# Performance work log

Hardware: AMD Instinct MI355X
Metric: run time of the kernel (lower is better)

Reference implementation:

```python
import jax, jax.numpy as jnp
import numpy as np

NUM_HEADS = 16
NUM_BUCKETS = 32
MAX_DISTANCE = 128


def _relative_position_bucket(relative_position, num_buckets=NUM_BUCKETS, max_distance=MAX_DISTANCE):
    # bidirectional=True (encoder self-attention)
    nb = num_buckets // 2  # 16
    buckets = (relative_position > 0).astype(jnp.int32) * nb
    rp = jnp.abs(relative_position)
    max_exact = nb // 2  # 8
    is_small = rp < max_exact
    # log-spaced bins for large distances; clamp arg of log to >=1 to avoid log(0)
    rp_f = jnp.maximum(rp, 1).astype(jnp.float32)
    large = max_exact + (
        jnp.log(rp_f / max_exact) / np.log(max_distance / max_exact) * (nb - max_exact)
    ).astype(jnp.int32)
    large = jnp.minimum(large, nb - 1)
    return buckets + jnp.where(is_small, rp, large)


def setup_inputs() -> dict:
    key = jax.random.key(0)
    ks = jax.random.split(key, 6)
    B, L, D = 2, 2048, 1024
    scale = 0.02  # keep activations in a sane range
    return {
        "hidden_states": jax.random.normal(ks[0], (B, L, D), dtype=jnp.float32),
        "Wq": jax.random.normal(ks[1], (D, D), dtype=jnp.float32) * scale,
        "Wk": jax.random.normal(ks[2], (D, D), dtype=jnp.float32) * scale,
        "Wv": jax.random.normal(ks[3], (D, D), dtype=jnp.float32) * scale,
        "Wo": jax.random.normal(ks[4], (D, D), dtype=jnp.float32) * scale,
        "bias_table": jax.random.normal(ks[5], (NUM_BUCKETS, NUM_HEADS), dtype=jnp.float32),
    }


def reference(hidden_states, Wq, Wk, Wv, Wo, bias_table):
    B, L, D = hidden_states.shape
    H = NUM_HEADS
    hd = D // H

    # projections (nn.Linear: y = x @ W.T), split heads -> [B, H, L, hd]
    def proj(x, W):
        return (x @ W.T).reshape(B, L, H, hd).transpose(0, 2, 1, 3)

    q = proj(hidden_states, Wq)
    k = proj(hidden_states, Wk)
    v = proj(hidden_states, Wv)

    # T5 relative position bias: [1, H, L, L]
    ctx = jnp.arange(L)[:, None]
    mem = jnp.arange(L)[None, :]
    buckets = _relative_position_bucket(mem - ctx)  # [L, L]
    position_bias = bias_table[buckets].transpose(2, 0, 1)[None]  # [1, H, L, L]

    # NOTE: T5-style attention has NO 1/sqrt(hd) scaling
    scores = jnp.einsum("bhqd,bhkd->bhqk", q, k) + position_bias
    attn = jax.nn.softmax(scores.astype(jnp.float32), axis=-1).astype(scores.dtype)
    out = jnp.einsum("bhqk,bhkd->bhqd", attn, v)
    out = out.transpose(0, 2, 1, 3).reshape(B, L, D)
    out = out @ Wo.T
    return out, position_bias
```

## Files before the change

kernel.cpp:

```cpp
#include <hip/hip_runtime.h>
#include <cstdint>
#include <cmath>

typedef unsigned short ushort_t;
typedef __bf16 bf16x8 __attribute__((ext_vector_type(8)));
typedef float f32x4 __attribute__((ext_vector_type(4)));
typedef ushort_t us4 __attribute__((ext_vector_type(4)));
typedef ushort_t us8 __attribute__((ext_vector_type(8)));

#define MFMA16(a, b, c) __builtin_amdgcn_mfma_f32_16x16x32_bf16(a, b, c, 0, 0, 0)
#define LOG2E 1.4426950408889634f

__device__ __forceinline__ ushort_t f2bf(float f) {
    union { __bf16 h; ushort_t u; } cv;
    cv.h = (__bf16)f;
    return cv.u;
}

__device__ __forceinline__ void glds16(const ushort_t* g, ushort_t* s) {
    __builtin_amdgcn_global_load_lds(
        (const __attribute__((address_space(1))) void*)(g),
        (__attribute__((address_space(3))) void*)(s), 16, 0, 0);
}

__global__ void cast_all_k(const float* __restrict__ x, const float* __restrict__ wq,
                           const float* __restrict__ wk, const float* __restrict__ wv,
                           const float* __restrict__ wo, ushort_t* __restrict__ xb,
                           ushort_t* __restrict__ wb, unsigned char* __restrict__ lut) {
    int id = blockIdx.x, t = threadIdx.x;
    if (id == 8192) {
        for (int idx = t; idx < 4095; idx += 256) {
            int rel = idx - 2047;
            int bb = (rel > 0) ? 16 : 0;
            int rp = (rel < 0) ? -rel : rel;
            int add;
            if (rp < 8) {
                add = rp;
            } else {
                float lg = (float)::log((double)rp * 0.125);
                double tt = ((double)lg) / 2.772588722239781 * 8.0;
                int large = 8 + (int)tt;
                add = (large < 15) ? large : 15;
            }
            lut[idx] = (unsigned char)(bb + add);
        }
        return;
    }
    const float* src;
    ushort_t* dst;
    int idx;
    float scale = 1.0f;
    if (id < 4096) {
        src = x; dst = xb; idx = id * 256 + t;
    } else {
        int r = (id - 4096) >> 10;
        idx = ((id - 4096) & 1023) * 256 + t;
        src = (r == 0) ? wq : (r == 1) ? wk : (r == 2) ? wv : wo;
        dst = wb + (size_t)r * 1048576;
        if (r == 0) scale = LOG2E;
    }
    float4 v = ((const float4*)src)[idx];
    us4 o;
    o.x = f2bf(v.x * scale); o.y = f2bf(v.y * scale);
    o.z = f2bf(v.z * scale); o.w = f2bf(v.w * scale);
    ((us4*)dst)[idx] = o;
}

template <int MODE>
__global__ __launch_bounds__(256) void gemm_bt_k(const ushort_t* __restrict__ A,
                                                 const ushort_t* __restrict__ B0,
                                                 void* __restrict__ C0,
                                                 int M, int N, int K, long sB, long sC) {
    __shared__ ushort_t As[128 * 64];
    __shared__ ushort_t Bs[128 * 64];
    const int tid = threadIdx.x;
    const int l = tid & 63, w = tid >> 6;
    const int quad = l >> 4, lc = l & 15;
    const int wm = w >> 1, wn = w & 1;
    const int m0 = blockIdx.y * 128, n0 = blockIdx.x * 128;
    const ushort_t* B = B0 + (long)blockIdx.z * sB;

    f32x4 acc[4][4] = {};
    const int rA = l >> 3;
    const int cA = ((l & 7) ^ rA) * 8;

    for (int k0 = 0; k0 < K; k0 += 64) {
#pragma unroll
        for (int t = 0; t < 4; ++t) {
            int row = w * 32 + t * 8;
            glds16(A + (size_t)(m0 + row + rA) * K + k0 + cA, &As[row * 64]);
            glds16(B + (size_t)(n0 + row + rA) * K + k0 + cA, &Bs[row * 64]);
        }
        __syncthreads();
#pragma unroll
        for (int ko = 0; ko < 2; ++ko) {
            const int ch = (((ko * 4 + quad) ^ (lc & 7))) * 8;
            bf16x8 af[4], bfr[4];
#pragma unroll
            for (int mt = 0; mt < 4; ++mt)
                af[mt] = *(const bf16x8*)&As[(wm * 64 + mt * 16 + lc) * 64 + ch];
#pragma unroll
            for (int nt = 0; nt < 4; ++nt)
                bfr[nt] = *(const bf16x8*)&Bs[(wn * 64 + nt * 16 + lc) * 64 + ch];
#pragma unroll
            for (int mt = 0; mt < 4; ++mt)
#pragma unroll
                for (int nt = 0; nt < 4; ++nt)
                    acc[mt][nt] = MFMA16(af[mt], bfr[nt], acc[mt][nt]);
        }
        __syncthreads();
    }
#pragma unroll
    for (int mt = 0; mt < 4; ++mt) {
#pragma unroll
        for (int nt = 0; nt < 4; ++nt) {
            int col = n0 + wn * 64 + nt * 16 + lc;
#pragma unroll
            for (int r = 0; r < 4; ++r) {
                int row = m0 + wm * 64 + mt * 16 + quad * 4 + r;
                if constexpr (MODE == 1) {
                    ((float*)C0)[(size_t)row * N + col] = acc[mt][nt][r];
                } else if constexpr (MODE == 0) {
                    (((ushort_t*)C0) + (long)blockIdx.z * sC)[(size_t)row * N + col] = f2bf(acc[mt][nt][r]);
                } else {
                    ((ushort_t*)C0)[(size_t)(col >> 11) * 2097152 + (size_t)row * 2048 + (col & 2047)] =
                        f2bf(acc[mt][nt][r]);
                }
            }
        }
    }
}

__global__ __launch_bounds__(256, 3) void attn_k(const ushort_t* __restrict__ Qg,
                                                 const ushort_t* __restrict__ Kg,
                                                 const ushort_t* __restrict__ VTg,
                                                 ushort_t* __restrict__ Ctx,
                                                 const unsigned char* __restrict__ lut,
                                                 const float* __restrict__ table,
                                                 float* __restrict__ bias_out) {
    __shared__ ushort_t Ks[128 * 64];
    __shared__ ushort_t VTs[64 * 128];
    __shared__ ushort_t QP[128 * 64];
    __shared__ float biasb[256];
    __shared__ float biasraw[256];

    const int tid = threadIdx.x, l = tid & 63, w = tid >> 6;
    const int quad = l >> 4, lc = l & 15;
    const int id = blockIdx.x;
    const int bh = id & 31, b = bh >> 4, h = bh & 15;
    const int q0 = (id >> 5) * 128;
    const size_t tokbase = (size_t)b * 2048;

    const int rK = l >> 3;
    const int cK = ((l & 7) ^ rK) * 8;
    const int rV = l >> 4;
    const int cVi = l & 15;

#pragma unroll
    for (int t = 0; t < 4; ++t) {
        int row0 = w * 32 + t * 8;
        glds16(Qg + (tokbase + q0 + row0 + rK) * 1024 + h * 64 + cK, &QP[row0 * 64]);
        glds16(Kg + (tokbase + row0 + rK) * 1024 + h * 64 + cK, &Ks[row0 * 64]);
    }
#pragma unroll
    for (int t = 0; t < 4; ++t) {
        int row0 = w * 16 + t * 4;
        int rsw = ((t & 1) * 4 + rV) & 7;
        int csw = (cVi & 8) | ((cVi & 7) ^ rsw);
        glds16(VTg + (size_t)(b * 1024 + h * 64 + row0 + rV) * 2048 + csw * 8, &VTs[row0 * 128]);
    }
    if (tid < 255) {
        float bvv = table[(int)lut[0 - q0 + tid + 1920] * 16 + h];
        biasraw[tid] = bvv;
        biasb[tid] = bvv * LOG2E;
    }
    __syncthreads();

    bf16x8 qf[2][2];
#pragma unroll
    for (int nt = 0; nt < 2; ++nt)
#pragma unroll
        for (int ko = 0; ko < 2; ++ko) {
            int row = w * 32 + nt * 16 + lc;
            int ch = ((ko * 4 + quad) ^ (lc & 7)) * 8;
            qf[nt][ko] = *(const bf16x8*)&QP[row * 64 + ch];
        }
    __syncthreads();

    float mstate[2] = {-1e30f, -1e30f};
    float lstate[2] = {0.f, 0.f};
    f32x4 acco[4][2] = {};
    ushort_t* Pw = &QP[w * 1280];
    const int cb0 = quad * 4 - (w * 32 + lc) + 127;
    const int cxor = lc & 3;

    const int bjf = (tid & 15) * 4 + b * 64;
    const int big = tid >> 4;

    for (int kt = 0; kt < 16; ++kt) {
        const int j0 = kt * 128;
        f32x4 accs[8][2] = {};
#pragma unroll
        for (int ko = 0; ko < 2; ++ko) {
            const int ch = ((ko * 4 + quad) ^ (lc & 7)) * 8;
#pragma unroll
            for (int mt = 0; mt < 8; ++mt) {
                bf16x8 kf = *(const bf16x8*)&Ks[(mt * 16 + lc) * 64 + ch];
                accs[mt][0] = MFMA16(kf, qf[0][ko], accs[mt][0]);
                accs[mt][1] = MFMA16(kf, qf[1][ko], accs[mt][1]);
            }
        }
        {
            float* outp = bias_out + ((size_t)h * 2048 + q0) * 2048 + j0;
#pragma unroll
            for (int rr = 0; rr < 8; ++rr) {
                int il = big + 16 * rr;
                int d0 = bjf - il + 127;
                f32x4 v;
                v[0] = biasraw[d0]; v[1] = biasraw[d0 + 1];
                v[2] = biasraw[d0 + 2]; v[3] = biasraw[d0 + 3];
                __builtin_nontemporal_store(v, (f32x4*)(outp + (size_t)il * 2048 + bjf));
            }
        }
        f32x4 bvp;
#pragma unroll
        for (int r = 0; r < 4; ++r) bvp[r] = biasb[cb0 - 16 + r];
#pragma unroll
        for (int mt = 0; mt < 8; ++mt) {
            f32x4 bvc;
#pragma unroll
            for (int r = 0; r < 4; ++r) bvc[r] = biasb[cb0 + mt * 16 + r];
            accs[mt][0] += bvc;
            accs[mt][1] += bvp;
            bvp = bvc;
        }
#pragma unroll
        for (int nt = 0; nt < 2; ++nt) {
            float mx = accs[0][nt][0];
#pragma unroll
            for (int mt = 0; mt < 8; ++mt)
#pragma unroll
                for (int r = 0; r < 4; ++r) mx = fmaxf(mx, accs[mt][nt][r]);
            mx = fmaxf(mx, __shfl_xor(mx, 16, 64));
            mx = fmaxf(mx, __shfl_xor(mx, 32, 64));
            float mo = mstate[nt], mn = fmaxf(mo, mx);
            float alpha = __builtin_amdgcn_exp2f(mo - mn);
            mstate[nt] = mn;
            float rs = 0.f;
#pragma unroll
            for (int mt = 0; mt < 8; ++mt)
#pragma unroll
                for (int r = 0; r < 4; ++r) {
                    float p = __builtin_amdgcn_exp2f(accs[mt][nt][r] - mn);
                    accs[mt][nt][r] = p;
                    rs += p;
                }
            rs += __shfl_xor(rs, 16, 64);
            rs += __shfl_xor(rs, 32, 64);
            lstate[nt] = lstate[nt] * alpha + rs;
#pragma unroll
            for (int dt = 0; dt < 4; ++dt) acco[dt][nt] *= alpha;
        }
#pragma unroll
        for (int kk = 0; kk < 4; ++kk) {
#pragma unroll
            for (int half = 0; half < 2; ++half) {
                int mt = kk * 2 + half;
                int c = half * 2 + (quad >> 1);
                int coff = ((c ^ cxor) * 8 + (quad & 1) * 4);
#pragma unroll
                for (int nt = 0; nt < 2; ++nt) {
                    us4 o;
#pragma unroll
                    for (int r = 0; r < 4; ++r) o[r] = f2bf(accs[mt][nt][r]);
                    *(us4*)&Pw[(nt * 16 + lc) * 40 + coff] = o;
                }
            }
            bf16x8 pf[2];
#pragma unroll
            for (int nt = 0; nt < 2; ++nt)
                pf[nt] = *(const bf16x8*)&Pw[(nt * 16 + lc) * 40 + (quad ^ cxor) * 8];
            bf16x8 vf[4];
#pragma unroll
            for (int dt = 0; dt < 4; ++dt) {
                int ch = kk * 4 + quad;
                int chs = ((ch & 8) | ((ch & 7) ^ (lc & 7))) * 8;
                vf[dt] = *(const bf16x8*)&VTs[(dt * 16 + lc) * 128 + chs];
            }
#pragma unroll
            for (int dt = 0; dt < 4; ++dt)
#pragma unroll
                for (int nt = 0; nt < 2; ++nt)
                    acco[dt][nt] = MFMA16(vf[dt], pf[nt], acco[dt][nt]);
        }
        __syncthreads();
        if (kt < 15) {
            const int jn = j0 + 128;
#pragma unroll
            for (int t = 0; t < 4; ++t) {
                int row0 = w * 32 + t * 8;
                glds16(Kg + (tokbase + jn + row0 + rK) * 1024 + h * 64 + cK, &Ks[row0 * 64]);
            }
#pragma unroll
            for (int t = 0; t < 4; ++t) {
                int row0 = w * 16 + t * 4;
                int rsw = ((t & 1) * 4 + rV) & 7;
                int csw = (cVi & 8) | ((cVi & 7) ^ rsw);
                glds16(VTg + (size_t)(b * 1024 + h * 64 + row0 + rV) * 2048 + jn + csw * 8,
                       &VTs[row0 * 128]);
            }
            if (tid < 255) {
                float bvv = table[(int)lut[jn - q0 + tid + 1920] * 16 + h];
                biasraw[tid] = bvv;
                biasb[tid] = bvv * LOG2E;
            }
            __syncthreads();
        }
    }
#pragma unroll
    for (int nt = 0; nt < 2; ++nt) {
        float inv = 1.0f / lstate[nt];
        size_t row = tokbase + q0 + w * 32 + nt * 16 + lc;
#pragma unroll
        for (int dt = 0; dt < 4; ++dt) {
            us4 o;
#pragma unroll
            for (int r = 0; r < 4; ++r) o[r] = f2bf(acco[dt][nt][r] * inv);
            *(us4*)&Ctx[row * 1024 + h * 64 + dt * 16 + quad * 4] = o;
        }
    }
}

extern "C" void kernel_launch(void* const* d_in, const int* in_sizes, int n_in,
                              void* d_out, int out_size, void* d_ws, size_t ws_size,
                              hipStream_t stream) {
    const float* hidden = (const float*)d_in[0];
    const float* Wq = (const float*)d_in[1];
    const float* Wk = (const float*)d_in[2];
    const float* Wv = (const float*)d_in[3];
    const float* Wo = (const float*)d_in[4];
    const float* table = (const float*)d_in[5];

    char* ws = (char*)d_ws;
    ushort_t* Xb  = (ushort_t*)(ws);
    ushort_t* Wb  = (ushort_t*)(ws + 8388608);
    ushort_t* Qg  = (ushort_t*)(ws + 16777216);
    ushort_t* Kgp = (ushort_t*)(ws + 25165824);
    ushort_t* VTg = (ushort_t*)(ws + 33554432);
    ushort_t* Ctx = (ushort_t*)(ws + 41943040);
    unsigned char* lutp = (unsigned char*)(ws + 50331648);

    float* out0 = (float*)d_out;
    float* out1 = out0 + 4194304;

    cast_all_k<<<8193, 256, 0, stream>>>(hidden, Wq, Wk, Wv, Wo, Xb, Wb, lutp);

    gemm_bt_k<0><<<dim3(8, 32, 2), 256, 0, stream>>>(Xb, Wb, (void*)Qg,
                                                     4096, 1024, 1024, 1048576, 4194304);
    gemm_bt_k<2><<<dim3(32, 8, 1), 256, 0, stream>>>(Wb + 2097152, Xb, (void*)VTg,
                                                     1024, 4096, 1024, 0, 0);
    attn_k<<<dim3(512), 256, 0, stream>>>(Qg, Kgp, VTg, Ctx, lutp, table, out1);
    gemm_bt_k<1><<<dim3(8, 32, 1), 256, 0, stream>>>(Ctx, Wb + 3145728, (void*)out0,
                                                     4096, 1024, 1024, 0, 0);
}
```

Baseline: 461.9 us.

## Double-buffer K tiles, load V fragments directly from global, single sync per tile

The attention kernel now double-buffers K tiles and the per-tile bias diagonal in shared memory, so loads for the next tile are issued before computing the current one. That replaces the two barriers per iteration with one. V^T fragments are read straight from global memory into registers at the start of each tile instead of being staged through LDS. The LOG2E scaling is folded into fmaf. Occupancy hint drops from 3 to 2 blocks per SM, and the direct global V loads add register pressure and latency exposure.

```diff
diff --git a/kernel.cpp b/kernel.cpp
--- a/kernel.cpp
+++ b/kernel.cpp
@@ -131,18 +131,16 @@
     }
 }
 
-__global__ __launch_bounds__(256, 3) void attn_k(const ushort_t* __restrict__ Qg,
+__global__ __launch_bounds__(256, 2) void attn_k(const ushort_t* __restrict__ Qg,
                                                  const ushort_t* __restrict__ Kg,
                                                  const ushort_t* __restrict__ VTg,
                                                  ushort_t* __restrict__ Ctx,
                                                  const unsigned char* __restrict__ lut,
                                                  const float* __restrict__ table,
                                                  float* __restrict__ bias_out) {
-    __shared__ ushort_t Ks[128 * 64];
-    __shared__ ushort_t VTs[64 * 128];
-    __shared__ ushort_t QP[128 * 64];
-    __shared__ float biasb[256];
-    __shared__ float biasraw[256];
+    __shared__ ushort_t Kbuf[2][128 * 64];
+    __shared__ ushort_t Pws[4 * 32 * 40];
+    __shared__ float diag[2][256];
 
     const int tid = threadIdx.x, l = tid & 63, w = tid >> 6;
     const int quad = l >> 4, lc = l & 15;
@@ -153,27 +151,14 @@
 
     const int rK = l >> 3;
     const int cK = ((l & 7) ^ rK) * 8;
-    const int rV = l >> 4;
-    const int cVi = l & 15;
 
 #pragma unroll
     for (int t = 0; t < 4; ++t) {
         int row0 = w * 32 + t * 8;
-        glds16(Qg + (tokbase + q0 + row0 + rK) * 1024 + h * 64 + cK, &QP[row0 * 64]);
-        glds16(Kg + (tokbase + row0 + rK) * 1024 + h * 64 + cK, &Ks[row0 * 64]);
-    }
-#pragma unroll
-    for (int t = 0; t < 4; ++t) {
-        int row0 = w * 16 + t * 4;
-        int rsw = ((t & 1) * 4 + rV) & 7;
-        int csw = (cVi & 8) | ((cVi & 7) ^ rsw);
-        glds16(VTg + (size_t)(b * 1024 + h * 64 + row0 + rV) * 2048 + csw * 8, &VTs[row0 * 128]);
-    }
-    if (tid < 255) {
-        float bvv = table[(int)lut[0 - q0 + tid + 1920] * 16 + h];
-        biasraw[tid] = bvv;
-        biasb[tid] = bvv * LOG2E;
-    }
+        glds16(Qg + (tokbase + q0 + row0 + rK) * 1024 + h * 64 + cK, &Kbuf[1][row0 * 64]);
+        glds16(Kg + (tokbase + row0 + rK) * 1024 + h * 64 + cK, &Kbuf[0][row0 * 64]);
+    }
+    if (tid < 255) diag[0][tid] = table[(int)lut[tid + 1920 - q0] * 16 + h];
     __syncthreads();
 
     bf16x8 qf[2][2];
@@ -183,33 +168,45 @@
         for (int ko = 0; ko < 2; ++ko) {
             int row = w * 32 + nt * 16 + lc;
             int ch = ((ko * 4 + quad) ^ (lc & 7)) * 8;
-            qf[nt][ko] = *(const bf16x8*)&QP[row * 64 + ch];
+            qf[nt][ko] = *(const bf16x8*)&Kbuf[1][row * 64 + ch];
         }
     __syncthreads();
 
     float mstate[2] = {-1e30f, -1e30f};
     float lstate[2] = {0.f, 0.f};
     f32x4 acco[4][2] = {};
-    ushort_t* Pw = &QP[w * 1280];
+    ushort_t* Pw = &Pws[w * 1280];
     const int cb0 = quad * 4 - (w * 32 + lc) + 127;
     const int cxor = lc & 3;
+    const ushort_t* VTbase = VTg + (size_t)(b * 1024 + h * 64) * 2048;
 
     const int bjf = (tid & 15) * 4 + b * 64;
     const int big = tid >> 4;
 
     for (int kt = 0; kt < 16; ++kt) {
         const int j0 = kt * 128;
-        f32x4 accs[8][2] = {};
-#pragma unroll
-        for (int ko = 0; ko < 2; ++ko) {
-            const int ch = ((ko * 4 + quad) ^ (lc & 7)) * 8;
-#pragma unroll
-            for (int mt = 0; mt < 8; ++mt) {
-                bf16x8 kf = *(const bf16x8*)&Ks[(mt * 16 + lc) * 64 + ch];
-                accs[mt][0] = MFMA16(kf, qf[0][ko], accs[mt][0]);
-                accs[mt][1] = MFMA16(kf, qf[1][ko], accs[mt][1]);
-            }
-        }
+        const int cur = kt & 1, nxt = cur ^ 1;
+        const ushort_t* Kc = Kbuf[cur];
+        const float* dc = diag[cur];
+
+        if (kt < 15) {
+            const int jn = j0 + 128;
+#pragma unroll
+            for (int t = 0; t < 4; ++t) {
+                int row0 = w * 32 + t * 8;
+                glds16(Kg + (tokbase + jn + row0 + rK) * 1024 + h * 64 + cK, &Kbuf[nxt][row0 * 64]);
+            }
+            if (tid < 255) diag[nxt][tid] = table[(int)lut[jn - q0 + tid + 1920] * 16 + h];
+        }
+
+        bf16x8 vf[4][4];
+#pragma unroll
+        for (int kk = 0; kk < 4; ++kk)
+#pragma unroll
+            for (int dt = 0; dt < 4; ++dt)
+                vf[kk][dt] = *(const bf16x8*)(VTbase + (size_t)(dt * 16 + lc) * 2048 +
+                                              j0 + kk * 32 + quad * 8);
+
         {
             float* outp = bias_out + ((size_t)h * 2048 + q0) * 2048 + j0;
 #pragma unroll
@@ -217,23 +214,39 @@
                 int il = big + 16 * rr;
                 int d0 = bjf - il + 127;
                 f32x4 v;
-                v[0] = biasraw[d0]; v[1] = biasraw[d0 + 1];
-                v[2] = biasraw[d0 + 2]; v[3] = biasraw[d0 + 3];
+                v[0] = dc[d0]; v[1] = dc[d0 + 1]; v[2] = dc[d0 + 2]; v[3] = dc[d0 + 3];
                 __builtin_nontemporal_store(v, (f32x4*)(outp + (size_t)il * 2048 + bjf));
             }
         }
-        f32x4 bvp;
-#pragma unroll
-        for (int r = 0; r < 4; ++r) bvp[r] = biasb[cb0 - 16 + r];
+
+        f32x4 accs[8][2] = {};
+#pragma unroll
+        for (int ko = 0; ko < 2; ++ko) {
+            const int ch = ((ko * 4 + quad) ^ (lc & 7)) * 8;
+#pragma unroll
+            for (int mt = 0; mt < 8; ++mt) {
+                bf16x8 kf = *(const bf16x8*)&Kc[(mt * 16 + lc) * 64 + ch];
+                accs[mt][0] = MFMA16(kf, qf[0][ko], accs[mt][0]);
+                accs[mt][1] = MFMA16(kf, qf[1][ko], accs[mt][1]);
+            }
+        }
+
+        float dprev[4], dcur[4];
+#pragma unroll
+        for (int r = 0; r < 4; ++r) dprev[r] = dc[cb0 - 16 + r];
 #pragma unroll
         for (int mt = 0; mt < 8; ++mt) {
-            f32x4 bvc;
-#pragma unroll
-            for (int r = 0; r < 4; ++r) bvc[r] = biasb[cb0 + mt * 16 + r];
-            accs[mt][0] += bvc;
-            accs[mt][1] += bvp;
-            bvp = bvc;
-        }
+#pragma unroll
+            for (int r = 0; r < 4; ++r) dcur[r] = dc[cb0 + mt * 16 + r];
+#pragma unroll
+            for (int r = 0; r < 4; ++r) {
+                accs[mt][0][r] = fmaf(dcur[r], LOG2E, accs[mt][0][r]);
+                accs[mt][1][r] = fmaf(dprev[r], LOG2E, accs[mt][1][r]);
+            }
+#pragma unroll
+            for (int r = 0; r < 4; ++r) dprev[r] = dcur[r];
+        }
+
 #pragma unroll
         for (int nt = 0; nt < 2; ++nt) {
             float mx = accs[0][nt][0];
@@ -261,6 +274,7 @@
 #pragma unroll
             for (int dt = 0; dt < 4; ++dt) acco[dt][nt] *= alpha;
         }
+
 #pragma unroll
         for (int kk = 0; kk < 4; ++kk) {
 #pragma unroll
@@ -280,43 +294,15 @@
 #pragma unroll
             for (int nt = 0; nt < 2; ++nt)
                 pf[nt] = *(const bf16x8*)&Pw[(nt * 16 + lc) * 40 + (quad ^ cxor) * 8];
-            bf16x8 vf[4];
-#pragma unroll
-            for (int dt = 0; dt < 4; ++dt) {
-                int ch = kk * 4 + quad;
-                int chs = ((ch & 8) | ((ch & 7) ^ (lc & 7))) * 8;
-                vf[dt] = *(const bf16x8*)&VTs[(dt * 16 + lc) * 128 + chs];
-            }
 #pragma unroll
             for (int dt = 0; dt < 4; ++dt)
 #pragma unroll
                 for (int nt = 0; nt < 2; ++nt)
-                    acco[dt][nt] = MFMA16(vf[dt], pf[nt], acco[dt][nt]);
-        }
-        __syncthreads();
-        if (kt < 15) {
-            const int jn = j0 + 128;
-#pragma unroll
-            for (int t = 0; t < 4; ++t) {
-                int row0 = w * 32 + t * 8;
-                glds16(Kg + (tokbase + jn + row0 + rK) * 1024 + h * 64 + cK, &Ks[row0 * 64]);
-            }
-#pragma unroll
-            for (int t = 0; t < 4; ++t) {
-                int row0 = w * 16 + t * 4;
-                int rsw = ((t & 1) * 4 + rV) & 7;
-                int csw = (cVi & 8) | ((cVi & 7) ^ rsw);
-                glds16(VTg + (size_t)(b * 1024 + h * 64 + row0 + rV) * 2048 + jn + csw * 8,
-                       &VTs[row0 * 128]);
-            }
-            if (tid < 255) {
-                float bvv = table[(int)lut[jn - q0 + tid + 1920] * 16 + h];
-                biasraw[tid] = bvv;
-                biasb[tid] = bvv * LOG2E;
-            }
-            __syncthreads();
-        }
-    }
+                    acco[dt][nt] = MFMA16(vf[kk][dt], pf[nt], acco[dt][nt]);
+        }
+        if (kt < 15) __syncthreads();
+    }
+
 #pragma unroll
     for (int nt = 0; nt < 2; ++nt) {
         float inv = 1.0f / lstate[nt];
```

Result: faster. 426.8 us (-7.6%).
